# Performance work log

Hardware: AMD Instinct MI355X
Metric: run time of the kernel (lower is better)

The kernel has to match this reference:

```python
import jax, jax.numpy as jnp
import numpy as np

# Static config (matches init_kwargs)
VOCAB, EMBED, HIDDEN = 32000, 256, 512
SLOTS, MEM_DIM, HEADS, TOPK = 1024, 64, 4, 8
B, T = 16, 128
# beta_read/beta_write are learned scalars but the torch forward detaches them
# via .item(); treat as constants (|beta| + 1e-6 with beta init ~1.0).
BETA_R = 1.0 + 1e-6
BETA_W = 1.0 + 1e-6
EPS = 1e-8


def setup_inputs() -> dict:
    key = jax.random.key(0)
    ks = jax.random.split(key, 16)
    s = 0.02
    HD = HEADS * MEM_DIM
    return {
        "input_seq": jax.random.randint(ks[0], (B, T), 0, VOCAB),
        "E": jax.random.normal(ks[1], (VOCAB, EMBED), jnp.float32) * s,
        "W_ih": jax.random.normal(ks[2], (4 * HIDDEN, EMBED + MEM_DIM), jnp.float32) * s,
        "W_hh": jax.random.normal(ks[3], (4 * HIDDEN, HIDDEN), jnp.float32) * s,
        "b_ih": jnp.zeros((4 * HIDDEN,), jnp.float32),
        "b_hh": jnp.zeros((4 * HIDDEN,), jnp.float32),
        "W_out": jax.random.normal(ks[4], (HIDDEN, VOCAB), jnp.float32) * s,
        "b_out": jnp.zeros((VOCAB,), jnp.float32),
        "W_rk": jax.random.normal(ks[5], (HIDDEN, HD), jnp.float32) * s,
        "b_rk": jnp.zeros((HD,), jnp.float32),
        "W_wk": jax.random.normal(ks[6], (HIDDEN, HD), jnp.float32) * s,
        "b_wk": jnp.zeros((HD,), jnp.float32),
        "W_wv": jax.random.normal(ks[7], (HIDDEN, HD), jnp.float32) * s,
        "b_wv": jnp.zeros((HD,), jnp.float32),
        "W_er": jax.random.normal(ks[8], (HIDDEN, HD), jnp.float32) * s,
        "b_er": jnp.zeros((HD,), jnp.float32),
    }


def _address(memory, keys, beta):
    # memory: [B,S,D], keys: [B,H,D] -> sparse (top-k) content weights [B,H,S]
    mem_n = memory / (jnp.linalg.norm(memory, axis=-1, keepdims=True) + EPS)
    key_n = keys / (jnp.linalg.norm(keys, axis=-1, keepdims=True) + EPS)
    scores = beta * jnp.einsum("bhd,bsd->bhs", key_n, mem_n)
    vals, idx = jax.lax.top_k(scores, TOPK)           # [B,H,K]
    sm = jax.nn.softmax(vals, axis=-1)                # softmax over top-k only
    w = jnp.zeros_like(scores)
    b_ix = jnp.arange(scores.shape[0])[:, None, None]
    h_ix = jnp.arange(HEADS)[None, :, None]
    return w.at[b_ix, h_ix, idx].set(sm)              # [B,H,S]


def reference(input_seq, E, W_ih, W_hh, b_ih, b_hh, W_out, b_out,
              W_rk, b_rk, W_wk, b_wk, W_wv, b_wv, W_er, b_er):
    Bq = input_seq.shape[0]
    memory0 = jnp.full((Bq, SLOTS, MEM_DIM), 1e-6, jnp.float32)
    h0 = jnp.zeros((Bq, HIDDEN), jnp.float32)
    c0 = jnp.zeros((Bq, HIDDEN), jnp.float32)
    r0 = jnp.zeros((Bq, MEM_DIM), jnp.float32)

    def step(carry, x_t):
        memory, h, c, read_vec = carry
        emb = E[x_t]                                          # [B,embed]
        inp = jnp.concatenate([emb, read_vec], axis=-1)
        gates = inp @ W_ih.T + b_ih + h @ W_hh.T + b_hh       # [B,4H]
        i, f, g, o = jnp.split(gates, 4, axis=-1)             # torch LSTM order
        c = jax.nn.sigmoid(f) * c + jax.nn.sigmoid(i) * jnp.tanh(g)
        h = jax.nn.sigmoid(o) * jnp.tanh(c)
        logits = h @ W_out + b_out                            # [B,V]
        rk = (h @ W_rk + b_rk).reshape(Bq, HEADS, MEM_DIM)
        wk = (h @ W_wk + b_wk).reshape(Bq, HEADS, MEM_DIM)
        wv = (h @ W_wv + b_wv).reshape(Bq, HEADS, MEM_DIM)
        er = jax.nn.sigmoid(h @ W_er + b_er).reshape(Bq, HEADS, MEM_DIM)
        # content-addressed top-k read
        rw = _address(memory, rk, BETA_R)                     # [B,H,S]
        read_vec = jnp.einsum("bhs,bsd->bhd", rw, memory).mean(axis=1)
        # erase + add write
        ww = _address(memory, wk, BETA_W)                     # [B,H,S]
        keep = jnp.prod(1.0 - ww[..., None] * er[:, :, None, :], axis=1)
        add = jnp.einsum("bhs,bhd->bsd", ww, wv)
        memory = memory * keep + add
        return (memory, h, c, read_vec), logits

    _, logits_seq = jax.lax.scan(step, (memory0, h0, c0, r0), input_seq.T)
    return jnp.transpose(logits_seq, (1, 0, 2))               # [B,T,V]
```

## Files before the change

kernel.cpp:

```cpp
#include <hip/hip_runtime.h>
#include <hip/hip_bf16.h>
#include <stdint.h>

typedef unsigned int uint;
typedef unsigned long long u64;

#define T_STEPS 128
#define BQ 16
#define HID 512
#define NSLOT 1024
#define MD 64
#define VOCAB 32000
#define BETA 1.000001f
#define EPSN 1e-8f

#define NB_PROJ 128
#define NB_BATCH 16
#define NB_REC (NB_PROJ + NB_BATCH)
#define GEMM_MT 16
#define GEMM_NT 500
#define NB_GEMM (GEMM_MT*GEMM_NT)

#define F_H(b) (((b))*32)
#define F_T(b) ((16+(b))*32)
#define F_K(w) ((32+(w))*32)
#define F_G(w) ((160+(w))*32)
#define NFLAGS 288

#define AL4(dst, p) asm volatile("global_load_dwordx4 %0, %1, off sc0 sc1" : "=v"(dst) : "v"(p))
#define AWAIT() do { asm volatile("s_waitcnt vmcnt(0)" ::: "memory"); __builtin_amdgcn_sched_barrier(0); } while(0)

__device__ __forceinline__ float sigm(float x){ return 1.f/(1.f+expf(-x)); }
__device__ __forceinline__ void astoref(float* p, float v){
  __hip_atomic_store(p, v, __ATOMIC_RELAXED, __HIP_MEMORY_SCOPE_AGENT);
}
__device__ __forceinline__ void astoreu32(uint* p, uint v){
  __hip_atomic_store(p, v, __ATOMIC_RELAXED, __HIP_MEMORY_SCOPE_AGENT);
}
__device__ __forceinline__ uint aloadu32(const uint* p){
  return __hip_atomic_load((uint*)p, __ATOMIC_RELAXED, __HIP_MEMORY_SCOPE_AGENT);
}
__device__ __forceinline__ void poll1(const uint* p, uint gen){
  while (aloadu32(p) < gen) __builtin_amdgcn_s_sleep(1);
}
__device__ __forceinline__ void poll64(const uint* p, uint gen){
  while (aloadu32(p) < gen) __builtin_amdgcn_s_sleep(64);
}
__device__ __forceinline__ void arrive1(uint* line, uint gen){
  asm volatile("s_waitcnt vmcnt(0)" ::: "memory");
  __syncthreads();
  if (threadIdx.x == 0) astoreu32(line, gen);
}

__device__ __forceinline__ u64 packsc(float v, int slot){
  uint u = __float_as_uint(v);
  u = (u & 0x80000000u) ? ~u : (u | 0x80000000u);
  return ((u64)u << 10) | (u64)(1023 - slot);
}
__device__ __forceinline__ float unpackval(u64 p){
  uint u = (uint)(p >> 10);
  uint bits = (u & 0x80000000u) ? (u & 0x7fffffffu) : ~u;
  return __uint_as_float(bits);
}
__device__ __forceinline__ int unpackslot(u64 p){ return 1023 - (int)(p & 1023u); }

__global__ __launch_bounds__(256) void prep_emb(const float* __restrict__ E,
                                                const int* __restrict__ seq,
                                                float* __restrict__ EMB){
  int m = blockIdx.x, t = m >> 4, b = m & 15;
  int x = seq[b*T_STEPS + t];
  EMB[(size_t)m*256 + threadIdx.x] = E[(size_t)x*256 + threadIdx.x];
}

__global__ __launch_bounds__(256) void gemm_emb(const float* __restrict__ A,
                                                const float* __restrict__ W_ih,
                                                const float* __restrict__ b_ih,
                                                const float* __restrict__ b_hh,
                                                float* __restrict__ C){
  __shared__ __align__(16) float As[16*68];
  __shared__ __align__(16) float Bs[16*68];
  int mt = blockIdx.x & 31, nt = blockIdx.x >> 5;
  int m0 = mt*64, n0 = nt*64;
  int tx = threadIdx.x & 15, ty = threadIdx.x >> 4;
  float acc[4][4] = {};
  for (int k0 = 0; k0 < 256; k0 += 16){
    int mm = threadIdx.x >> 2, kq = (threadIdx.x & 3)*4;
    float4 a = *(const float4*)(A + (size_t)(m0+mm)*256 + k0 + kq);
    As[(kq+0)*68+mm]=a.x; As[(kq+1)*68+mm]=a.y; As[(kq+2)*68+mm]=a.z; As[(kq+3)*68+mm]=a.w;
    int pp = n0 + mm;
    int r = (pp & 3)*512 + (pp >> 2);
    float4 bv = *(const float4*)(W_ih + (size_t)r*320 + k0 + kq);
    Bs[(kq+0)*68+mm]=bv.x; Bs[(kq+1)*68+mm]=bv.y; Bs[(kq+2)*68+mm]=bv.z; Bs[(kq+3)*68+mm]=bv.w;
    __syncthreads();
    #pragma unroll
    for (int kk = 0; kk < 16; ++kk){
      float4 av = *(const float4*)(As + kk*68 + ty*4);
      float4 bb = *(const float4*)(Bs + kk*68 + tx*4);
      float aa[4] = {av.x,av.y,av.z,av.w};
      float bv2[4] = {bb.x,bb.y,bb.z,bb.w};
      #pragma unroll
      for (int i = 0; i < 4; ++i)
        #pragma unroll
        for (int j = 0; j < 4; ++j)
          acc[i][j] = fmaf(aa[i], bv2[j], acc[i][j]);
    }
    __syncthreads();
  }
  #pragma unroll
  for (int i = 0; i < 4; ++i){
    int m = m0 + ty*4 + i;
    #pragma unroll
    for (int j = 0; j < 4; ++j){
      int pp = n0 + tx*4 + j;
      int r = (pp & 3)*512 + (pp >> 2);
      C[(size_t)m*2048 + pp] = acc[i][j] + b_ih[r] + b_hh[r];
    }
  }
}

__global__ __launch_bounds__(256) void make_wrvT(const float* __restrict__ W_ih,
                                                 float* __restrict__ WT){
  int idx = blockIdx.x*256 + threadIdx.x;
  int k = idx >> 11, p = idx & 2047;
  int r = (p & 3)*512 + (p >> 2);
  WT[idx] = W_ih[(size_t)r*320 + 256 + k];
}

__global__ __launch_bounds__(256, 2) void mega_kernel(
    const float* __restrict__ W_hh, const float* __restrict__ WT,
    const float* __restrict__ W_rk, const float* __restrict__ b_rk,
    const float* __restrict__ W_wk, const float* __restrict__ b_wk,
    const float* __restrict__ W_wv, const float* __restrict__ b_wv,
    const float* __restrict__ W_er, const float* __restrict__ b_er,
    const float* __restrict__ G_emb, float* __restrict__ H_all,
    float* __restrict__ mem_row, float* __restrict__ memT,
    float* __restrict__ projbuf, float* __restrict__ gp_g,
    const float* __restrict__ W_out, const float* __restrict__ b_out,
    float* __restrict__ C_out, uint* __restrict__ arrv)
{
  __shared__ __align__(16) float smem[12384];
  const int tid = threadIdx.x;
  const int wg  = blockIdx.x;

  if (wg < NB_PROJ){
    float* hs = smem;
    float* Ws = smem + 8256;
    const int p1_b = tid >> 4, p1_col = tid & 15;
    const int pcol = wg*16 + p1_col;
    const int rrow = (pcol & 3)*512 + (pcol >> 2);
    const int msel = wg >> 5, col0 = (wg & 31)*8;
    const float* Wm  = (msel==0)? W_rk : (msel==1)? W_wk : (msel==2)? W_wv : W_er;
    const float* bmp = (msel==0)? b_rk : (msel==1)? b_wk : (msel==2)? b_wv : b_er;
    for (int i = tid; i < 8*HID; i += 256){
      int k = i >> 3, j = i & 7;
      Ws[j*516 + k] = Wm[(size_t)k*256 + col0 + j];
    }
    #pragma clang loop unroll(disable)
    for (int t = 0; t < T_STEPS-1; ++t){
      if (tid < 16) poll1(arrv + F_H(tid), (uint)(t+1));
      __syncthreads();
      const float4* hsrc = (const float4*)(H_all + (size_t)t*BQ*HID);
      for (int i = tid; i < 2048; i += 256){
        int b = i >> 7, q = i & 127;
        *(float4*)(hs + b*516 + q*4) = hsrc[i];
      }
      __syncthreads();
      {
        int b = tid >> 4, o2 = (tid & 15) >> 1, half = tid & 1;
        const float4* wp = (const float4*)(Ws + o2*516 + half*256);
        const float4* xp = (const float4*)(hs + b*516 + half*256);
        float a0 = 0.f, a1 = 0.f;
        #pragma unroll 4
        for (int k = 0; k < 64; k += 2){
          float4 w = wp[k], x = xp[k];
          a0=fmaf(w.x,x.x,a0); a0=fmaf(w.y,x.y,a0); a0=fmaf(w.z,x.z,a0); a0=fmaf(w.w,x.w,a0);
          w = wp[k+1]; x = xp[k+1];
          a1=fmaf(w.x,x.x,a1); a1=fmaf(w.y,x.y,a1); a1=fmaf(w.z,x.z,a1); a1=fmaf(w.w,x.w,a1);
        }
        float acc = a0 + a1;
        float other = __shfl_xor(acc, 1);
        if (half == 0){
          float v = acc + other + bmp[col0 + o2];
          if (msel == 3) v = sigm(v);
          astoref(projbuf + (size_t)b*1024 + msel*256 + col0 + o2, v);
        }
      }
      arrive1(arrv + F_K(wg), (uint)(t+1));
      {
        float a0 = G_emb[(size_t)((t+1)*BQ + p1_b)*2048 + pcol];
        float a1 = 0.f, a2 = 0.f, a3 = 0.f;
        const float4* wh = (const float4*)(W_hh + (size_t)rrow*HID);
        const float4* xv = (const float4*)(hs + p1_b*516);
        #pragma unroll 2
        for (int k = 0; k < 128; k += 4){
          float4 w, x;
          w=wh[k+0]; x=xv[k+0]; a0=fmaf(w.x,x.x,a0); a0=fmaf(w.y,x.y,a0); a0=fmaf(w.z,x.z,a0); a0=fmaf(w.w,x.w,a0);
          w=wh[k+1]; x=xv[k+1]; a1=fmaf(w.x,x.x,a1); a1=fmaf(w.y,x.y,a1); a1=fmaf(w.z,x.z,a1); a1=fmaf(w.w,x.w,a1);
          w=wh[k+2]; x=xv[k+2]; a2=fmaf(w.x,x.x,a2); a2=fmaf(w.y,x.y,a2); a2=fmaf(w.z,x.z,a2); a2=fmaf(w.w,x.w,a2);
          w=wh[k+3]; x=xv[k+3]; a3=fmaf(w.x,x.x,a3); a3=fmaf(w.y,x.y,a3); a3=fmaf(w.z,x.z,a3); a3=fmaf(w.w,x.w,a3);
        }
        astoref(gp_g + (size_t)p1_b*2048 + pcol, (a0+a1)+(a2+a3));
      }
      arrive1(arrv + F_G(wg), (uint)(t+1));
    }
  } else if (wg < NB_REC){
    const int b = wg - NB_PROJ;
    float* keyT  = smem;
    float* wv_s  = smem + 512;
    float* er_s  = smem + 768;
    float* rv_s  = smem + 1024;
    float* rvp   = smem + 1088;
    float* wgt   = smem + 2112;
    int*   slotl = (int*)(smem + 2176);
    int*   ge_s  = (int*)(smem + 2240);
    float* knrm  = smem + 2272;
    u64*   cnd   = (u64*)(smem + 2280);
    float* mrow = mem_row + (size_t)b*NSLOT*MD;
    float* mT   = memT    + (size_t)b*MD*NSLOT;

    {
      float4 iv = make_float4(1e-6f,1e-6f,1e-6f,1e-6f);
      for (int i = tid; i < NSLOT*MD/4; i += 256){
        *(float4*)(mrow + (size_t)i*4) = iv;
        *(float4*)(mT   + (size_t)i*4) = iv;
      }
    }
    float c0 = 0.f, c1 = 0.f;
    {
      float4 gA = *(const float4*)(G_emb + (size_t)b*2048 + tid*8);
      float4 gB = *(const float4*)(G_emb + (size_t)b*2048 + tid*8 + 4);
      c0 = sigm(gA.x)*tanhf(gA.z);
      float h0v = sigm(gA.w)*tanhf(c0);
      c1 = sigm(gB.x)*tanhf(gB.z);
      float h1v = sigm(gB.w)*tanhf(c1);
      astoref(H_all + (size_t)b*HID + tid*2,     h0v);
      astoref(H_all + (size_t)b*HID + tid*2 + 1, h1v);
    }
    asm volatile("s_waitcnt vmcnt(0)" ::: "memory");
    __syncthreads();
    if (tid == 0){ astoreu32(arrv + F_H(b), 1u); astoreu32(arrv + F_T(b), 1u); }

    const int lane = tid & 63, wv_id = tid >> 6;
    #pragma clang loop unroll(disable)
    for (int t = 0; t < T_STEPS-1; ++t){
      if (tid < 128) poll1(arrv + F_K(tid), (uint)(t+1));
      __syncthreads();
      {
        float4 v; AL4(v, (const float4*)(projbuf + (size_t)b*1024) + tid); AWAIT();
        if (tid < 128){
          int q = tid*4;
          keyT[((q+0)&63)*8 + ((q+0)>>6)] = v.x;
          keyT[((q+1)&63)*8 + ((q+1)>>6)] = v.y;
          keyT[((q+2)&63)*8 + ((q+2)>>6)] = v.z;
          keyT[((q+3)&63)*8 + ((q+3)>>6)] = v.w;
        } else {
          *(float4*)(wv_s + (tid-128)*4) = v;
        }
      }
      __syncthreads();
      if (tid < 8){
        float kn = 0.f;
        #pragma unroll 8
        for (int d = 0; d < 64; ++d){ float kv = keyT[d*8 + tid]; kn = fmaf(kv,kv,kn); }
        knrm[tid] = 1.f / (sqrtf(kn) + EPSN);
      }
      float ss0=0,ss1=0,ss2=0,ss3=0;
      float sc[8][4] = {};
      {
        const float* mp = mT + tid;
        #pragma unroll 2
        for (int d = 0; d < 64; ++d){
          float4 ka = *(const float4*)(keyT + d*8);
          float4 kb = *(const float4*)(keyT + d*8 + 4);
          float m0 = mp[d*1024], m1 = mp[d*1024+256], m2 = mp[d*1024+512], m3 = mp[d*1024+768];
          ss0=fmaf(m0,m0,ss0); ss1=fmaf(m1,m1,ss1); ss2=fmaf(m2,m2,ss2); ss3=fmaf(m3,m3,ss3);
          sc[0][0]=fmaf(m0,ka.x,sc[0][0]); sc[0][1]=fmaf(m1,ka.x,sc[0][1]); sc[0][2]=fmaf(m2,ka.x,sc[0][2]); sc[0][3]=fmaf(m3,ka.x,sc[0][3]);
          sc[1][0]=fmaf(m0,ka.y,sc[1][0]); sc[1][1]=fmaf(m1,ka.y,sc[1][1]); sc[1][2]=fmaf(m2,ka.y,sc[1][2]); sc[1][3]=fmaf(m3,ka.y,sc[1][3]);
          sc[2][0]=fmaf(m0,ka.z,sc[2][0]); sc[2][1]=fmaf(m1,ka.z,sc[2][1]); sc[2][2]=fmaf(m2,ka.z,sc[2][2]); sc[2][3]=fmaf(m3,ka.z,sc[2][3]);
          sc[3][0]=fmaf(m0,ka.w,sc[3][0]); sc[3][1]=fmaf(m1,ka.w,sc[3][1]); sc[3][2]=fmaf(m2,ka.w,sc[3][2]); sc[3][3]=fmaf(m3,ka.w,sc[3][3]);
          sc[4][0]=fmaf(m0,kb.x,sc[4][0]); sc[4][1]=fmaf(m1,kb.x,sc[4][1]); sc[4][2]=fmaf(m2,kb.x,sc[4][2]); sc[4][3]=fmaf(m3,kb.x,sc[4][3]);
          sc[5][0]=fmaf(m0,kb.y,sc[5][0]); sc[5][1]=fmaf(m1,kb.y,sc[5][1]); sc[5][2]=fmaf(m2,kb.y,sc[5][2]); sc[5][3]=fmaf(m3,kb.y,sc[5][3]);
          sc[6][0]=fmaf(m0,kb.z,sc[6][0]); sc[6][1]=fmaf(m1,kb.z,sc[6][1]); sc[6][2]=fmaf(m2,kb.z,sc[6][2]); sc[6][3]=fmaf(m3,kb.z,sc[6][3]);
          sc[7][0]=fmaf(m0,kb.w,sc[7][0]); sc[7][1]=fmaf(m1,kb.w,sc[7][1]); sc[7][2]=fmaf(m2,kb.w,sc[7][2]); sc[7][3]=fmaf(m3,kb.w,sc[7][3]);
        }
      }
      float rn0 = BETA/(sqrtf(ss0)+EPSN), rn1 = BETA/(sqrtf(ss1)+EPSN);
      float rn2 = BETA/(sqrtf(ss2)+EPSN), rn3 = BETA/(sqrtf(ss3)+EPSN);
      #pragma unroll
      for (int key = 0; key < 8; ++key){
        u64 p0 = packsc(sc[key][0]*rn0, tid);
        u64 p1 = packsc(sc[key][1]*rn1, tid+256);
        u64 p2 = packsc(sc[key][2]*rn2, tid+512);
        u64 p3 = packsc(sc[key][3]*rn3, tid+768);
        #pragma unroll
        for (int r = 0; r < 8; ++r){
          u64 m01 = p0 > p1 ? p0 : p1;
          u64 m23 = p2 > p3 ? p2 : p3;
          u64 m = m01 > m23 ? m01 : m23;
          #pragma unroll
          for (int o = 32; o; o >>= 1){ u64 q = __shfl_xor(m, o); if (q > m) m = q; }
          if (p0 == m) p0 = 0; else if (p1 == m) p1 = 0;
          else if (p2 == m) p2 = 0; else if (p3 == m) p3 = 0;
          if (lane == 0) cnd[(key*4 + wv_id)*8 + r] = m;
        }
      }
      __syncthreads();
      if (tid < 8){
        const u64* cl = cnd + tid*32;
        int i0=0,i1=0,i2=0,i3=0;
        float vals[8]; int sl[8];
        #pragma unroll
        for (int r = 0; r < 8; ++r){
          u64 a = cl[i0], bb2 = cl[8+i1], c = cl[16+i2], d = cl[24+i3];
          u64 m1_ = a > bb2 ? a : bb2;
          u64 m2_ = c > d ? c : d;
          u64 m = m1_ > m2_ ? m1_ : m2_;
          if (m == a) ++i0; else if (m == bb2) ++i1; else if (m == c) ++i2; else ++i3;
          vals[r] = unpackval(m) * knrm[tid];
          sl[r]   = unpackslot(m);
        }
        float vm = vals[0], et[8], sum = 0.f;
        #pragma unroll
        for (int r = 0; r < 8; ++r){ et[r] = expf(vals[r]-vm); sum += et[r]; }
        float rs = 1.f/sum;
        #pragma unroll
        for (int r = 0; r < 8; ++r){ wgt[tid*8+r] = et[r]*rs; slotl[tid*8+r] = sl[r]; }
      }
      __syncthreads();
      #pragma unroll
      for (int jj = 0; jj < 4; ++jj){
        int it = tid + 256*jj;
        int hh = it >> 8, rr = (it >> 6) & 3, d = it & 63;
        float w0 = wgt[hh*8+rr],   w1 = wgt[hh*8+rr+4];
        int   s0 = slotl[hh*8+rr], s1 = slotl[hh*8+rr+4];
        rvp[it] = w0*mrow[(size_t)s0*64+d] + w1*mrow[(size_t)s1*64+d];
      }
      if (tid < 32){
        int me = slotl[32+tid], g = tid;
        for (int e = 0; e < 32; ++e){ if (e < tid && slotl[32+e] == me){ g = e; break; } }
        ge_s[tid] = g;
      }
      __syncthreads();
      if (tid < 64){
        float s = 0.f;
        #pragma unroll
        for (int i = 0; i < 16; ++i) s += rvp[i*64 + tid];
        rv_s[tid] = 0.25f*s;
      }
      #pragma unroll
      for (int jj = 0; jj < 8; ++jj){
        int it = tid + 256*jj;
        int g = it >> 6, d = it & 63;
        if (ge_s[g] == g){
          float keep = 1.f, add = 0.f;
          for (int e = 0; e < 32; ++e){
            if (ge_s[e] == g){
              float w = wgt[32+e]; int h = e >> 3;
              keep *= (1.f - w*er_s[h*64+d]);
              add  += w*wv_s[h*64+d];
            }
          }
          int slot = slotl[32+g];
          float nv = mrow[(size_t)slot*64+d]*keep + add;
          mrow[(size_t)slot*64+d] = nv;
          mT[(size_t)d*1024+slot] = nv;
        }
      }
      __syncthreads();
      if (tid < 128) poll1(arrv + F_G(tid), (uint)(t+1));
      __syncthreads();
      float ga0,ga1,ga2,ga3,ga4,ga5,ga6,ga7;
      {
        float4 g0, g1;
        AL4(g0, (const float4*)(gp_g + (size_t)b*2048 + tid*8));
        AL4(g1, (const float4*)(gp_g + (size_t)b*2048 + tid*8 + 4));
        AWAIT();
        ga0=g0.x; ga1=g0.y; ga2=g0.z; ga3=g0.w; ga4=g1.x; ga5=g1.y; ga6=g1.z; ga7=g1.w;
      }
      {
        const float4* wt = (const float4*)(WT + tid*8);
        #pragma unroll 4
        for (int d = 0; d < 64; ++d){
          float r = rv_s[d];
          float4 w0 = wt[d*512], w1 = wt[d*512 + 1];
          ga0=fmaf(r,w0.x,ga0); ga1=fmaf(r,w0.y,ga1); ga2=fmaf(r,w0.z,ga2); ga3=fmaf(r,w0.w,ga3);
          ga4=fmaf(r,w1.x,ga4); ga5=fmaf(r,w1.y,ga5); ga6=fmaf(r,w1.z,ga6); ga7=fmaf(r,w1.w,ga7);
        }
      }
      c0 = sigm(ga1)*c0 + sigm(ga0)*tanhf(ga2);
      float h0v = sigm(ga3)*tanhf(c0);
      c1 = sigm(ga5)*c1 + sigm(ga4)*tanhf(ga6);
      float h1v = sigm(ga7)*tanhf(c1);
      astoref(H_all + (size_t)((t+1)*BQ + b)*HID + tid*2,     h0v);
      astoref(H_all + (size_t)((t+1)*BQ + b)*HID + tid*2 + 1, h1v);
      asm volatile("s_waitcnt vmcnt(0)" ::: "memory");
      __syncthreads();
      if (tid == 0){ astoreu32(arrv + F_H(b), (uint)(t+2)); astoreu32(arrv + F_T(b), (uint)(t+2)); }
    }
  } else {
    int gb = wg - NB_REC;
    int mt = gb / GEMM_NT, nt = gb - mt*GEMM_NT;
    int m0 = mt*128, n0 = nt*64;
    uint need = (uint)(mt*8 + 8);
    if (tid < 16) poll64(arrv + F_T(tid), need);
    __syncthreads();
    float* As = smem;
    float* Bs = smem + 2112;
    int tx = tid & 15, ty = tid >> 4;
    float acc[8][4] = {};
    for (int k0 = 0; k0 < 512; k0 += 16){
      int mm = tid >> 1, kq = (tid & 1)*8;
      float4 a0 = *(const float4*)(H_all + (size_t)(m0+mm)*512 + k0 + kq);
      float4 a1 = *(const float4*)(H_all + (size_t)(m0+mm)*512 + k0 + kq + 4);
      As[(kq+0)*132+mm]=a0.x; As[(kq+1)*132+mm]=a0.y; As[(kq+2)*132+mm]=a0.z; As[(kq+3)*132+mm]=a0.w;
      As[(kq+4)*132+mm]=a1.x; As[(kq+5)*132+mm]=a1.y; As[(kq+6)*132+mm]=a1.z; As[(kq+7)*132+mm]=a1.w;
      int kk2 = tid >> 4, nq = (tid & 15)*4;
      *(float4*)(Bs + kk2*64 + nq) = *(const float4*)(W_out + (size_t)(k0+kk2)*VOCAB + n0 + nq);
      __syncthreads();
      #pragma unroll
      for (int kk = 0; kk < 16; ++kk){
        float4 x0 = *(const float4*)(As + kk*132 + ty*8);
        float4 x1 = *(const float4*)(As + kk*132 + ty*8 + 4);
        float4 bv = *(const float4*)(Bs + kk*64 + tx*4);
        float aa[8] = {x0.x,x0.y,x0.z,x0.w,x1.x,x1.y,x1.z,x1.w};
        float bb[4] = {bv.x,bv.y,bv.z,bv.w};
        #pragma unroll
        for (int i = 0; i < 8; ++i)
          #pragma unroll
          for (int j = 0; j < 4; ++j)
            acc[i][j] = fmaf(aa[i], bb[j], acc[i][j]);
      }
      __syncthreads();
    }
    #pragma unroll
    for (int i = 0; i < 8; ++i){
      int m = m0 + ty*8 + i;
      int bq = m & 15, tt = m >> 4;
      float* crow = C_out + ((size_t)bq*T_STEPS + tt)*VOCAB + n0 + tx*4;
      #pragma unroll
      for (int j = 0; j < 4; ++j) crow[j] = acc[i][j] + b_out[n0 + tx*4 + j];
    }
  }
}

extern "C" void kernel_launch(void* const* d_in, const int* in_sizes, int n_in,
                              void* d_out, int out_size, void* d_ws, size_t ws_size,
                              hipStream_t stream){
  const int*   seq   = (const int*)d_in[0];
  const float* E     = (const float*)d_in[1];
  const float* W_ih  = (const float*)d_in[2];
  const float* W_hh  = (const float*)d_in[3];
  const float* b_ih  = (const float*)d_in[4];
  const float* b_hh  = (const float*)d_in[5];
  const float* W_out = (const float*)d_in[6];
  const float* b_out = (const float*)d_in[7];
  const float* W_rk  = (const float*)d_in[8];
  const float* b_rk  = (const float*)d_in[9];
  const float* W_wk  = (const float*)d_in[10];
  const float* b_wk  = (const float*)d_in[11];
  const float* W_wv  = (const float*)d_in[12];
  const float* b_wv  = (const float*)d_in[13];
  const float* W_er  = (const float*)d_in[14];
  const float* b_er  = (const float*)d_in[15];
  float* out = (float*)d_out;
  (void)in_sizes; (void)n_in; (void)out_size; (void)ws_size;

  char* ws = (char*)d_ws;
  size_t off = 0;
  auto alloc = [&](size_t bytes) -> void* {
    off = (off + 255) & ~(size_t)255;
    void* p = ws + off;
    off += bytes;
    return p;
  };
  float* EMB     = (float*)alloc((size_t)2048*256*4);
  float* G_emb   = (float*)alloc((size_t)2048*2048*4);
  float* H_all   = (float*)alloc((size_t)2048*512*4);
  float* mem_row = (float*)alloc((size_t)16*1024*64*4);
  float* memT    = (float*)alloc((size_t)16*64*1024*4);
  float* projbuf = (float*)alloc((size_t)16*1024*4);
  float* gp_g    = (float*)alloc((size_t)16*2048*4);
  float* WT      = (float*)alloc((size_t)64*2048*4);
  uint*  arrv    = (uint*)alloc((size_t)NFLAGS*32*4);

  hipMemsetAsync(arrv, 0, (size_t)NFLAGS*32*4, stream);
  prep_emb<<<2048, 256, 0, stream>>>(E, seq, EMB);
  gemm_emb<<<1024, 256, 0, stream>>>(EMB, W_ih, b_ih, b_hh, G_emb);
  make_wrvT<<<512, 256, 0, stream>>>(W_ih, WT);
  mega_kernel<<<NB_REC + NB_GEMM, 256, 0, stream>>>(
      W_hh, WT, W_rk, b_rk, W_wk, b_wk, W_wv, b_wv, W_er, b_er,
      G_emb, H_all, mem_row, memT, projbuf, gp_g,
      W_out, b_out, out, arrv);
}
```

Before: 7.825 ms.

## Split output GEMM out of persistent mega kernel into separate launch

Moves the vocabulary projection GEMM out of the persistent mega kernel, where its blocks polled per-timestep flags to overlap with the recurrence, into a standalone kernel launched after the recurrence finishes. This removes the polling blocks that compete with the recurrent blocks for CUs and memory bandwidth and may slow the latency-critical serial loop. The cost is giving up the overlap of the logits GEMM with the sequential recurrence, and the blockIdx mapping now puts M tiles on the fast index so they share W_out tiles.

Result: slower. 8.283 ms (+5.9%).

```diff
diff --git a/kernel.cpp b/kernel.cpp
--- a/kernel.cpp
+++ b/kernel.cpp
@@ -17,12 +17,8 @@
 #define NB_PROJ 128
 #define NB_BATCH 16
 #define NB_REC (NB_PROJ + NB_BATCH)
-#define GEMM_MT 16
-#define GEMM_NT 500
-#define NB_GEMM (GEMM_MT*GEMM_NT)
 
 #define F_H(b) (((b))*32)
-#define F_T(b) ((16+(b))*32)
 #define F_K(w) ((32+(w))*32)
 #define F_G(w) ((160+(w))*32)
 #define NFLAGS 288
@@ -42,9 +38,6 @@
 }
 __device__ __forceinline__ void poll1(const uint* p, uint gen){
   while (aloadu32(p) < gen) __builtin_amdgcn_s_sleep(1);
-}
-__device__ __forceinline__ void poll64(const uint* p, uint gen){
-  while (aloadu32(p) < gen) __builtin_amdgcn_s_sleep(64);
 }
 __device__ __forceinline__ void arrive1(uint* line, uint gen){
   asm volatile("s_waitcnt vmcnt(0)" ::: "memory");
@@ -126,7 +119,7 @@
   WT[idx] = W_ih[(size_t)r*320 + 256 + k];
 }
 
-__global__ __launch_bounds__(256, 2) void mega_kernel(
+__global__ __launch_bounds__(256, 2) void recur_kernel(
     const float* __restrict__ W_hh, const float* __restrict__ WT,
     const float* __restrict__ W_rk, const float* __restrict__ b_rk,
     const float* __restrict__ W_wk, const float* __restrict__ b_wk,
@@ -135,8 +128,7 @@
     const float* __restrict__ G_emb, float* __restrict__ H_all,
     float* __restrict__ mem_row, float* __restrict__ memT,
     float* __restrict__ projbuf, float* __restrict__ gp_g,
-    const float* __restrict__ W_out, const float* __restrict__ b_out,
-    float* __restrict__ C_out, uint* __restrict__ arrv)
+    uint* __restrict__ arrv)
 {
   __shared__ __align__(16) float smem[12384];
   const int tid = threadIdx.x;
@@ -238,7 +230,7 @@
     }
     asm volatile("s_waitcnt vmcnt(0)" ::: "memory");
     __syncthreads();
-    if (tid == 0){ astoreu32(arrv + F_H(b), 1u); astoreu32(arrv + F_T(b), 1u); }
+    if (tid == 0) astoreu32(arrv + F_H(b), 1u);
 
     const int lane = tid & 63, wv_id = tid >> 6;
     #pragma clang loop unroll(disable)
@@ -395,51 +387,52 @@
       astoref(H_all + (size_t)((t+1)*BQ + b)*HID + tid*2 + 1, h1v);
       asm volatile("s_waitcnt vmcnt(0)" ::: "memory");
       __syncthreads();
-      if (tid == 0){ astoreu32(arrv + F_H(b), (uint)(t+2)); astoreu32(arrv + F_T(b), (uint)(t+2)); }
-    }
-  } else {
-    int gb = wg - NB_REC;
-    int mt = gb / GEMM_NT, nt = gb - mt*GEMM_NT;
-    int m0 = mt*128, n0 = nt*64;
-    uint need = (uint)(mt*8 + 8);
-    if (tid < 16) poll64(arrv + F_T(tid), need);
+      if (tid == 0) astoreu32(arrv + F_H(b), (uint)(t+2));
+    }
+  }
+}
+
+__global__ __launch_bounds__(256) void gemm_out(const float* __restrict__ A,
+                                                const float* __restrict__ Bmat,
+                                                const float* __restrict__ bias,
+                                                float* __restrict__ C){
+  __shared__ __align__(16) float As[16*132];
+  __shared__ __align__(16) float Bs[16*64];
+  int mt = blockIdx.x & 15, nt = blockIdx.x >> 4;
+  int m0 = mt*128, n0 = nt*64;
+  int tx = threadIdx.x & 15, ty = threadIdx.x >> 4;
+  float acc[8][4] = {};
+  for (int k0 = 0; k0 < 512; k0 += 16){
+    int mm = threadIdx.x >> 1, kq = (threadIdx.x & 1)*8;
+    float4 a0 = *(const float4*)(A + (size_t)(m0+mm)*512 + k0 + kq);
+    float4 a1 = *(const float4*)(A + (size_t)(m0+mm)*512 + k0 + kq + 4);
+    As[(kq+0)*132+mm]=a0.x; As[(kq+1)*132+mm]=a0.y; As[(kq+2)*132+mm]=a0.z; As[(kq+3)*132+mm]=a0.w;
+    As[(kq+4)*132+mm]=a1.x; As[(kq+5)*132+mm]=a1.y; As[(kq+6)*132+mm]=a1.z; As[(kq+7)*132+mm]=a1.w;
+    int kk2 = threadIdx.x >> 4, nq = (threadIdx.x & 15)*4;
+    *(float4*)(Bs + kk2*64 + nq) = *(const float4*)(Bmat + (size_t)(k0+kk2)*VOCAB + n0 + nq);
     __syncthreads();
-    float* As = smem;
-    float* Bs = smem + 2112;
-    int tx = tid & 15, ty = tid >> 4;
-    float acc[8][4] = {};
-    for (int k0 = 0; k0 < 512; k0 += 16){
-      int mm = tid >> 1, kq = (tid & 1)*8;
-      float4 a0 = *(const float4*)(H_all + (size_t)(m0+mm)*512 + k0 + kq);
-      float4 a1 = *(const float4*)(H_all + (size_t)(m0+mm)*512 + k0 + kq + 4);
-      As[(kq+0)*132+mm]=a0.x; As[(kq+1)*132+mm]=a0.y; As[(kq+2)*132+mm]=a0.z; As[(kq+3)*132+mm]=a0.w;
-      As[(kq+4)*132+mm]=a1.x; As[(kq+5)*132+mm]=a1.y; As[(kq+6)*132+mm]=a1.z; As[(kq+7)*132+mm]=a1.w;
-      int kk2 = tid >> 4, nq = (tid & 15)*4;
-      *(float4*)(Bs + kk2*64 + nq) = *(const float4*)(W_out + (size_t)(k0+kk2)*VOCAB + n0 + nq);
-      __syncthreads();
+    #pragma unroll
+    for (int kk = 0; kk < 16; ++kk){
+      float4 x0 = *(const float4*)(As + kk*132 + ty*8);
+      float4 x1 = *(const float4*)(As + kk*132 + ty*8 + 4);
+      float4 bv = *(const float4*)(Bs + kk*64 + tx*4);
+      float aa[8] = {x0.x,x0.y,x0.z,x0.w,x1.x,x1.y,x1.z,x1.w};
+      float bb[4] = {bv.x,bv.y,bv.z,bv.w};
       #pragma unroll
-      for (int kk = 0; kk < 16; ++kk){
-        float4 x0 = *(const float4*)(As + kk*132 + ty*8);
-        float4 x1 = *(const float4*)(As + kk*132 + ty*8 + 4);
-        float4 bv = *(const float4*)(Bs + kk*64 + tx*4);
-        float aa[8] = {x0.x,x0.y,x0.z,x0.w,x1.x,x1.y,x1.z,x1.w};
-        float bb[4] = {bv.x,bv.y,bv.z,bv.w};
-        #pragma unroll
-        for (int i = 0; i < 8; ++i)
-          #pragma unroll
-          for (int j = 0; j < 4; ++j)
-            acc[i][j] = fmaf(aa[i], bb[j], acc[i][j]);
-      }
-      __syncthreads();
-    }
+      for (int i = 0; i < 8; ++i)
+        #pragma unroll
+        for (int j = 0; j < 4; ++j)
+          acc[i][j] = fmaf(aa[i], bb[j], acc[i][j]);
+    }
+    __syncthreads();
+  }
+  #pragma unroll
+  for (int i = 0; i < 8; ++i){
+    int m = m0 + ty*8 + i;
+    int bq = m & 15, tt = m >> 4;
+    float* crow = C + ((size_t)bq*T_STEPS + tt)*VOCAB + n0 + tx*4;
     #pragma unroll
-    for (int i = 0; i < 8; ++i){
-      int m = m0 + ty*8 + i;
-      int bq = m & 15, tt = m >> 4;
-      float* crow = C_out + ((size_t)bq*T_STEPS + tt)*VOCAB + n0 + tx*4;
-      #pragma unroll
-      for (int j = 0; j < 4; ++j) crow[j] = acc[i][j] + b_out[n0 + tx*4 + j];
-    }
+    for (int j = 0; j < 4; ++j) crow[j] = acc[i][j] + bias[n0 + tx*4 + j];
   }
 }
 
@@ -487,8 +480,8 @@
   prep_emb<<<2048, 256, 0, stream>>>(E, seq, EMB);
   gemm_emb<<<1024, 256, 0, stream>>>(EMB, W_ih, b_ih, b_hh, G_emb);
   make_wrvT<<<512, 256, 0, stream>>>(W_ih, WT);
-  mega_kernel<<<NB_REC + NB_GEMM, 256, 0, stream>>>(
+  recur_kernel<<<NB_REC, 256, 0, stream>>>(
       W_hh, WT, W_rk, b_rk, W_wk, b_wk, W_wv, b_wv, W_er, b_er,
-      G_emb, H_all, mem_row, memT, projbuf, gp_g,
-      W_out, b_out, out, arrv);
-}
+      G_emb, H_all, mem_row, memT, projbuf, gp_g, arrv);
+  gemm_out<<<16*500, 256, 0, stream>>>(H_all, W_out, b_out, out);
+}
```
